# Kernel optimization log

Measured on AMD Instinct MI355X. Metric: run time of the kernel, lower is better.

Reference implementation:

```python
import jax, jax.numpy as jnp
import numpy as np

B, L, PATCH_IN, D, NPOS = 64, 1024, 768, 1152, 256


def setup_inputs() -> dict:
    key = jax.random.key(0)
    k1, k2, k3, k4 = jax.random.split(key, 4)
    pixel_values = jax.random.normal(k1, (B, L, PATCH_IN), dtype=jnp.float32)
    # per-sample (h, w) with h*w <= L and h, w >= 16 (pure upsampling of 16x16 grid)
    hs = np.array([16 + (i % 17) for i in range(B)], dtype=np.int64)
    ws = (L // hs).astype(np.int64)
    spatial_shapes = jnp.asarray(np.stack([hs, ws], axis=1))
    W = jax.random.normal(k2, (D, PATCH_IN), dtype=jnp.float32) * 0.02
    b = jax.random.normal(k3, (D,), dtype=jnp.float32) * 0.02
    pos_emb = jax.random.normal(k4, (NPOS, D), dtype=jnp.float32) * 0.02
    return {"pixel_values": pixel_values, "spatial_shapes": spatial_shapes,
            "W": W, "b": b, "pos_emb": pos_emb}


def _resized_pos_embeddings(pos_emb, spatial_shapes_np, max_length):
    # pos_emb: [num_patches, D] -> [G, G, D] grid
    g = int(np.sqrt(pos_emb.shape[0]))
    d = pos_emb.shape[1]
    grid = pos_emb.reshape(g, g, d)
    rows = []
    for i in range(spatial_shapes_np.shape[0]):
        h, w = int(spatial_shapes_np[i, 0]), int(spatial_shapes_np[i, 1])
        # half-pixel bilinear == torch F.interpolate(align_corners=False); antialias
        # is a no-op for upsampling (h, w >= g)
        r = jax.image.resize(grid, (h, w, d), method="bilinear").reshape(h * w, d)
        pad = jnp.broadcast_to(r[0], (max_length - h * w, d))  # replicate first patch
        rows.append(jnp.concatenate([r, pad], axis=0))
    return jnp.stack(rows)  # [B, max_length, D]


def reference(pixel_values, spatial_shapes, W, b, pos_emb):
    # patch linear embedding: [B, L, Cpp] x [D, Cpp] -> [B, L, D]
    patch_embeds = jnp.einsum("blk,dk->bld", pixel_values, W) + b
    ss = np.asarray(spatial_shapes)  # static per-sample shapes
    pos = _resized_pos_embeddings(pos_emb, ss, pixel_values.shape[1])
    return patch_embeds + pos
```

## Files before the change

### kernel.cpp

```cpp
#include <hip/hip_runtime.h>

typedef __bf16 bf16x8 __attribute__((ext_vector_type(8)));
typedef float  f32x4  __attribute__((ext_vector_type(4)));

constexpr int BM = 128, BN = 128, BK = 32;
constexpr int MDIM = 65536, NDIM = 1152, KDIM = 768;
constexpr int NBN = NDIM / BN;
constexpr int NKT = KDIM / BK;
constexpr int GRID = (MDIM / BM) * NBN;
constexpr int LDSROWB = BK * 2;

__device__ __forceinline__ void gload16(const void* g, void* l) {
  __builtin_amdgcn_global_load_lds(
      (const __attribute__((address_space(1))) void*)g,
      (__attribute__((address_space(3))) void*)l, 16, 0, 0);
}

__device__ __forceinline__ unsigned pk2(float x, float y) {
  __bf16 a = (__bf16)x, b = (__bf16)y;
  return (unsigned)__builtin_bit_cast(unsigned short, a) |
         ((unsigned)__builtin_bit_cast(unsigned short, b) << 16);
}

__device__ __forceinline__ void epilogue(const f32x4 acc[4][4], int bm, int bn,
                                         int wr, int wc, int lane,
                                         const int* __restrict__ ss,
                                         const float* __restrict__ bias,
                                         const float* __restrict__ pos,
                                         float* __restrict__ out) {
  const int fr = lane & 15;
  const int kg = lane >> 4;
  const int colbase = bn * BN + wc * 64 + fr;
  float bvals[4];
#pragma unroll
  for (int nf = 0; nf < 4; ++nf) bvals[nf] = bias[colbase + nf * 16];

  const int s  = bm >> 3;
  const int h  = ss[2 * s];
  const int w  = ss[2 * s + 1];
  const int hw = h * w;
  const float rh = 16.0f / (float)h;
  const float rw = 16.0f / (float)w;

  const int row0 = bm * BM + wr * 64 + kg * 4;

#pragma unroll
  for (int mf = 0; mf < 4; ++mf) {
#pragma unroll
    for (int rg = 0; rg < 4; ++rg) {
      const int row = row0 + mf * 16 + rg;
      int p = row & 1023;
      if (p >= hw) p = 0;
      const int y = p / w;
      const int x = p - y * w;
      const float fy = ((float)y + 0.5f) * rh - 0.5f;
      const float fx = ((float)x + 0.5f) * rw - 0.5f;
      const float yf = floorf(fy), xf = floorf(fx);
      const float ty = fy - yf,   tx = fx - xf;
      int iy0 = (int)yf, ix0 = (int)xf;
      int iy1 = iy0 + 1 > 15 ? 15 : iy0 + 1;
      int ix1 = ix0 + 1 > 15 ? 15 : ix0 + 1;
      iy0 = iy0 < 0 ? 0 : iy0;
      ix0 = ix0 < 0 ? 0 : ix0;
      const float* g00 = pos + (size_t)(iy0 * 16 + ix0) * NDIM;
      const float* g01 = pos + (size_t)(iy0 * 16 + ix1) * NDIM;
      const float* g10 = pos + (size_t)(iy1 * 16 + ix0) * NDIM;
      const float* g11 = pos + (size_t)(iy1 * 16 + ix1) * NDIM;
      float* orow = out + (size_t)row * NDIM;
#pragma unroll
      for (int nf = 0; nf < 4; ++nf) {
        const int col = colbase + nf * 16;
        const float p00 = g00[col], p01 = g01[col];
        const float p10 = g10[col], p11 = g11[col];
        const float top = p00 + tx * (p01 - p00);
        const float bot = p10 + tx * (p11 - p10);
        const float pv  = top + ty * (bot - top);
        orow[col] = acc[mf][nf][rg] + bvals[nf] + pv;
      }
    }
  }
}

__global__ __launch_bounds__(256)
void cvt_bf16_kernel(const float* __restrict__ in, __bf16* __restrict__ out, int n8) {
  int i = blockIdx.x * blockDim.x + threadIdx.x;
  const int stride = gridDim.x * blockDim.x;
  for (; i < n8; i += stride) {
    const float4 a = reinterpret_cast<const float4*>(in)[2 * i];
    const float4 b = reinterpret_cast<const float4*>(in)[2 * i + 1];
    bf16x8 r;
    r[0] = (__bf16)a.x; r[1] = (__bf16)a.y; r[2] = (__bf16)a.z; r[3] = (__bf16)a.w;
    r[4] = (__bf16)b.x; r[5] = (__bf16)b.y; r[6] = (__bf16)b.z; r[7] = (__bf16)b.w;
    reinterpret_cast<bf16x8*>(out)[i] = r;
  }
}

__global__ __launch_bounds__(256, 2)
void gemm_pre_kernel(const __bf16* __restrict__ Ab,
                     const __bf16* __restrict__ Bb,
                     const int*   __restrict__ ss,
                     const float* __restrict__ bias,
                     const float* __restrict__ pos,
                     float* __restrict__ out) {
  __shared__ __bf16 As[2][BM * BK];
  __shared__ __bf16 Bs[2][BM * BK];

  const int tid  = threadIdx.x;
  const int lane = tid & 63;
  const int wid  = tid >> 6;
  const int wr   = wid >> 1;
  const int wc   = wid & 1;

  const int bidh = blockIdx.x;
  const int bid  = (bidh & 7) * (GRID / 8) + (bidh >> 3);
  const int bm   = bid / NBN;
  const int bn   = bid % NBN;

  const __bf16* Abase = Ab + (size_t)bm * BM * KDIM;
  const __bf16* Bbase = Bb + (size_t)bn * BN * KDIM;

  auto stage = [&](int kt, int buf) {
    const int ko = kt * BK;
#pragma unroll
    for (int i = 0; i < 2; ++i) {
      const int c   = i * 256 + tid;
      const int row = c >> 2;
      const int prt = c & 3;
      gload16(Abase + (size_t)row * KDIM + ko + prt * 8,
              (char*)(&As[buf][0]) + c * 16);
      gload16(Bbase + (size_t)row * KDIM + ko + prt * 8,
              (char*)(&Bs[buf][0]) + c * 16);
    }
  };

  f32x4 acc[4][4];
#pragma unroll
  for (int i = 0; i < 4; ++i)
#pragma unroll
    for (int j = 0; j < 4; ++j) acc[i][j] = (f32x4)0.0f;

  const int fr = lane & 15;
  const int kg = lane >> 4;
  const int abase = (wr * 64 + fr) * LDSROWB + kg * 16;
  const int bbase = (wc * 64 + fr) * LDSROWB + kg * 16;

  auto compute = [&](int buf) {
    const char* pa = reinterpret_cast<const char*>(&As[buf][0]);
    const char* pb = reinterpret_cast<const char*>(&Bs[buf][0]);
    bf16x8 af[4], bfv[4];
#pragma unroll
    for (int mf = 0; mf < 4; ++mf)
      af[mf] = *reinterpret_cast<const bf16x8*>(pa + abase + mf * 16 * LDSROWB);
#pragma unroll
    for (int nf = 0; nf < 4; ++nf)
      bfv[nf] = *reinterpret_cast<const bf16x8*>(pb + bbase + nf * 16 * LDSROWB);
#pragma unroll
    for (int mf = 0; mf < 4; ++mf)
#pragma unroll
      for (int nf = 0; nf < 4; ++nf)
        acc[mf][nf] = __builtin_amdgcn_mfma_f32_16x16x32_bf16(af[mf], bfv[nf], acc[mf][nf], 0, 0, 0);
  };

  stage(0, 0);
  for (int kt = 0; kt < NKT; ++kt) {
    const int cur = kt & 1;
    __syncthreads();
    if (kt + 1 < NKT) stage(kt + 1, cur ^ 1);
    compute(cur);
  }

  epilogue(acc, bm, bn, wr, wc, lane, ss, bias, pos, out);
}

__global__ __launch_bounds__(256, 2)
void gemm_fb_kernel(const float* __restrict__ A,
                    const int*   __restrict__ ss,
                    const float* __restrict__ Wm,
                    const float* __restrict__ bias,
                    const float* __restrict__ pos,
                    float* __restrict__ out) {
  __shared__ unsigned short As[2][BM * BK];
  __shared__ unsigned short Bs[2][BM * BK];

  const int tid  = threadIdx.x;
  const int lane = tid & 63;
  const int wid  = tid >> 6;
  const int wr   = wid >> 1;
  const int wc   = wid & 1;

  const int bidh = blockIdx.x;
  const int bid  = (bidh & 7) * (GRID / 8) + (bidh >> 3);
  const int bm   = bid / NBN;
  const int bn   = bid % NBN;

  const int srow0 = tid >> 3;
  const int skc   = tid & 7;
  const float* Ag = A  + (size_t)(bm * BM + srow0) * KDIM + skc * 4;
  const float* Bg = Wm + (size_t)(bn * BN + srow0) * KDIM + skc * 4;

  float4 ra[4], rb[4];

  auto stage_load = [&](int kt) {
    const int ko = kt * BK;
#pragma unroll
    for (int r = 0; r < 4; ++r) {
      ra[r] = *reinterpret_cast<const float4*>(Ag + (size_t)(r * 32) * KDIM + ko);
      rb[r] = *reinterpret_cast<const float4*>(Bg + (size_t)(r * 32) * KDIM + ko);
    }
  };

  auto stage_write = [&](int buf) {
#pragma unroll
    for (int r = 0; r < 4; ++r) {
      const int arow = r * 32 + srow0;
      int off = arow * LDSROWB + skc * 8;
      off ^= (arow & 7) << 4;
      uint2 pa, pb;
      pa.x = pk2(ra[r].x, ra[r].y); pa.y = pk2(ra[r].z, ra[r].w);
      pb.x = pk2(rb[r].x, rb[r].y); pb.y = pk2(rb[r].z, rb[r].w);
      *reinterpret_cast<uint2*>(reinterpret_cast<char*>(&As[buf][0]) + off) = pa;
      *reinterpret_cast<uint2*>(reinterpret_cast<char*>(&Bs[buf][0]) + off) = pb;
    }
  };

  f32x4 acc[4][4];
#pragma unroll
  for (int i = 0; i < 4; ++i)
#pragma unroll
    for (int j = 0; j < 4; ++j) acc[i][j] = (f32x4)0.0f;

  const int fr = lane & 15;
  const int kg = lane >> 4;
  int abase = (wr * 64 + fr) * LDSROWB + kg * 16; abase ^= (fr & 7) << 4;
  int bbase = (wc * 64 + fr) * LDSROWB + kg * 16; bbase ^= (fr & 7) << 4;

  auto compute = [&](int buf) {
    const char* pa = reinterpret_cast<const char*>(&As[buf][0]);
    const char* pb = reinterpret_cast<const char*>(&Bs[buf][0]);
    bf16x8 af[4], bfv[4];
#pragma unroll
    for (int mf = 0; mf < 4; ++mf)
      af[mf] = *reinterpret_cast<const bf16x8*>(pa + abase + mf * 16 * LDSROWB);
#pragma unroll
    for (int nf = 0; nf < 4; ++nf)
      bfv[nf] = *reinterpret_cast<const bf16x8*>(pb + bbase + nf * 16 * LDSROWB);
#pragma unroll
    for (int mf = 0; mf < 4; ++mf)
#pragma unroll
      for (int nf = 0; nf < 4; ++nf)
        acc[mf][nf] = __builtin_amdgcn_mfma_f32_16x16x32_bf16(af[mf], bfv[nf], acc[mf][nf], 0, 0, 0);
  };

  stage_load(0);
  stage_write(0);
  for (int kt = 0; kt < NKT; ++kt) {
    const int cur = kt & 1;
    if (kt + 1 < NKT) stage_load(kt + 1);
    __syncthreads();
    compute(cur);
    if (kt + 1 < NKT) stage_write(cur ^ 1);
  }

  epilogue(acc, bm, bn, wr, wc, lane, ss, bias, pos, out);
}

extern "C" void kernel_launch(void* const* d_in, const int* in_sizes, int n_in,
                              void* d_out, int out_size, void* d_ws, size_t ws_size,
                              hipStream_t stream) {
  const float* A    = (const float*)d_in[0];
  const int*   ss   = (const int*)d_in[1];
  const float* Wm   = (const float*)d_in[2];
  const float* bias = (const float*)d_in[3];
  const float* pos  = (const float*)d_in[4];
  float* out = (float*)d_out;

  const size_t needA = (size_t)MDIM * KDIM * 2;
  const size_t needW = (size_t)NDIM * KDIM * 2;

  if (ws_size >= needA + needW) {
    __bf16* Ab = (__bf16*)d_ws;
    __bf16* Bb = (__bf16*)((char*)d_ws + needA);
    cvt_bf16_kernel<<<2048, 256, 0, stream>>>(A, Ab, MDIM * KDIM / 8);
    cvt_bf16_kernel<<<432, 256, 0, stream>>>(Wm, Bb, NDIM * KDIM / 8);
    gemm_pre_kernel<<<GRID, 256, 0, stream>>>(Ab, Bb, ss, bias, pos, out);
  } else {
    gemm_fb_kernel<<<GRID, 256, 0, stream>>>(A, ss, Wm, bias, pos, out);
  }
}
```

Before: 292.8 us.

## Pre-swizzle operands into MFMA fragment layout and load fragments directly from global

The bf16 conversion kernels now write A and W in a fragment-major layout that matches the 16x16x32 MFMA operand layout, so each lane reads its bf16x8 fragment with one contiguous 16-byte global load. The GEMM kernel drops LDS staging and __syncthreads entirely, using register double-buffering across k-tiles instead. This removes LDS traffic and barriers, but each wave now fetches its own operands from global or L2, with no sharing through LDS between the waves of a block. Performance then depends on cache hit rate and on how well load latency is hidden.

```diff
diff --git a/kernel.cpp b/kernel.cpp
--- a/kernel.cpp
+++ b/kernel.cpp
@@ -10,11 +10,7 @@
 constexpr int GRID = (MDIM / BM) * NBN;
 constexpr int LDSROWB = BK * 2;
 
-__device__ __forceinline__ void gload16(const void* g, void* l) {
-  __builtin_amdgcn_global_load_lds(
-      (const __attribute__((address_space(1))) void*)g,
-      (__attribute__((address_space(3))) void*)l, 16, 0, 0);
-}
+constexpr int RSTRIDE = NKT * 64 * 8;
 
 __device__ __forceinline__ unsigned pk2(float x, float y) {
   __bf16 a = (__bf16)x, b = (__bf16)y;
@@ -82,29 +78,29 @@
 }
 
 __global__ __launch_bounds__(256)
-void cvt_bf16_kernel(const float* __restrict__ in, __bf16* __restrict__ out, int n8) {
-  int i = blockIdx.x * blockDim.x + threadIdx.x;
-  const int stride = gridDim.x * blockDim.x;
-  for (; i < n8; i += stride) {
-    const float4 a = reinterpret_cast<const float4*>(in)[2 * i];
-    const float4 b = reinterpret_cast<const float4*>(in)[2 * i + 1];
-    bf16x8 r;
-    r[0] = (__bf16)a.x; r[1] = (__bf16)a.y; r[2] = (__bf16)a.z; r[3] = (__bf16)a.w;
-    r[4] = (__bf16)b.x; r[5] = (__bf16)b.y; r[6] = (__bf16)b.z; r[7] = (__bf16)b.w;
-    reinterpret_cast<bf16x8*>(out)[i] = r;
-  }
+void cvt_frag_kernel(const float* __restrict__ in, __bf16* __restrict__ out) {
+  const int c   = blockIdx.x * 256 + threadIdx.x;
+  const int fr  = c & 15;
+  const int kg  = (c >> 4) & 3;
+  const int ktR = c >> 6;
+  const int kt  = ktR % NKT;
+  const int R   = ktR / NKT;
+  const float* src = in + (size_t)(R * 16 + fr) * KDIM + kt * 32 + kg * 8;
+  const float4 a = *reinterpret_cast<const float4*>(src);
+  const float4 b = *reinterpret_cast<const float4*>(src + 4);
+  bf16x8 r;
+  r[0] = (__bf16)a.x; r[1] = (__bf16)a.y; r[2] = (__bf16)a.z; r[3] = (__bf16)a.w;
+  r[4] = (__bf16)b.x; r[5] = (__bf16)b.y; r[6] = (__bf16)b.z; r[7] = (__bf16)b.w;
+  *reinterpret_cast<bf16x8*>(out + (size_t)c * 8) = r;
 }
 
 __global__ __launch_bounds__(256, 2)
-void gemm_pre_kernel(const __bf16* __restrict__ Ab,
-                     const __bf16* __restrict__ Bb,
-                     const int*   __restrict__ ss,
-                     const float* __restrict__ bias,
-                     const float* __restrict__ pos,
-                     float* __restrict__ out) {
-  __shared__ __bf16 As[2][BM * BK];
-  __shared__ __bf16 Bs[2][BM * BK];
-
+void gemm_frag_kernel(const __bf16* __restrict__ Aw,
+                      const __bf16* __restrict__ Bw,
+                      const int*   __restrict__ ss,
+                      const float* __restrict__ bias,
+                      const float* __restrict__ pos,
+                      float* __restrict__ out) {
   const int tid  = threadIdx.x;
   const int lane = tid & 63;
   const int wid  = tid >> 6;
@@ -116,22 +112,8 @@
   const int bm   = bid / NBN;
   const int bn   = bid % NBN;
 
-  const __bf16* Abase = Ab + (size_t)bm * BM * KDIM;
-  const __bf16* Bbase = Bb + (size_t)bn * BN * KDIM;
-
-  auto stage = [&](int kt, int buf) {
-    const int ko = kt * BK;
-#pragma unroll
-    for (int i = 0; i < 2; ++i) {
-      const int c   = i * 256 + tid;
-      const int row = c >> 2;
-      const int prt = c & 3;
-      gload16(Abase + (size_t)row * KDIM + ko + prt * 8,
-              (char*)(&As[buf][0]) + c * 16);
-      gload16(Bbase + (size_t)row * KDIM + ko + prt * 8,
-              (char*)(&Bs[buf][0]) + c * 16);
-    }
-  };
+  const __bf16* pA = Aw + (size_t)(bm * 8 + wr * 4) * RSTRIDE + lane * 8;
+  const __bf16* pB = Bw + (size_t)(bn * 8 + wc * 4) * RSTRIDE + lane * 8;
 
   f32x4 acc[4][4];
 #pragma unroll
@@ -139,34 +121,33 @@
 #pragma unroll
     for (int j = 0; j < 4; ++j) acc[i][j] = (f32x4)0.0f;
 
-  const int fr = lane & 15;
-  const int kg = lane >> 4;
-  const int abase = (wr * 64 + fr) * LDSROWB + kg * 16;
-  const int bbase = (wc * 64 + fr) * LDSROWB + kg * 16;
-
-  auto compute = [&](int buf) {
-    const char* pa = reinterpret_cast<const char*>(&As[buf][0]);
-    const char* pb = reinterpret_cast<const char*>(&Bs[buf][0]);
-    bf16x8 af[4], bfv[4];
-#pragma unroll
-    for (int mf = 0; mf < 4; ++mf)
-      af[mf] = *reinterpret_cast<const bf16x8*>(pa + abase + mf * 16 * LDSROWB);
+  bf16x8 a0[4], b0[4], a1[4], b1[4];
+
+  auto lda = [&](bf16x8* d, int kt) {
+#pragma unroll
+    for (int mf = 0; mf < 4; ++mf)
+      d[mf] = *reinterpret_cast<const bf16x8*>(pA + mf * RSTRIDE + kt * 512);
+  };
+  auto ldb = [&](bf16x8* d, int kt) {
 #pragma unroll
     for (int nf = 0; nf < 4; ++nf)
-      bfv[nf] = *reinterpret_cast<const bf16x8*>(pb + bbase + nf * 16 * LDSROWB);
+      d[nf] = *reinterpret_cast<const bf16x8*>(pB + nf * RSTRIDE + kt * 512);
+  };
+  auto mm = [&](const bf16x8* a, const bf16x8* b) {
 #pragma unroll
     for (int mf = 0; mf < 4; ++mf)
 #pragma unroll
       for (int nf = 0; nf < 4; ++nf)
-        acc[mf][nf] = __builtin_amdgcn_mfma_f32_16x16x32_bf16(af[mf], bfv[nf], acc[mf][nf], 0, 0, 0);
-  };
-
-  stage(0, 0);
-  for (int kt = 0; kt < NKT; ++kt) {
-    const int cur = kt & 1;
-    __syncthreads();
-    if (kt + 1 < NKT) stage(kt + 1, cur ^ 1);
-    compute(cur);
+        acc[mf][nf] = __builtin_amdgcn_mfma_f32_16x16x32_bf16(a[mf], b[nf], acc[mf][nf], 0, 0, 0);
+  };
+
+  lda(a0, 0); ldb(b0, 0);
+#pragma unroll
+  for (int kt = 0; kt < NKT; kt += 2) {
+    lda(a1, kt + 1); ldb(b1, kt + 1);
+    mm(a0, b0);
+    if (kt + 2 < NKT) { lda(a0, kt + 2); ldb(b0, kt + 2); }
+    mm(a1, b1);
   }
 
   epilogue(acc, bm, bn, wr, wc, lane, ss, bias, pos, out);
@@ -280,9 +261,11 @@
   if (ws_size >= needA + needW) {
     __bf16* Ab = (__bf16*)d_ws;
     __bf16* Bb = (__bf16*)((char*)d_ws + needA);
-    cvt_bf16_kernel<<<2048, 256, 0, stream>>>(A, Ab, MDIM * KDIM / 8);
-    cvt_bf16_kernel<<<432, 256, 0, stream>>>(Wm, Bb, NDIM * KDIM / 8);
-    gemm_pre_kernel<<<GRID, 256, 0, stream>>>(Ab, Bb, ss, bias, pos, out);
+    const int chunksA = MDIM / 16 * NKT * 64;
+    const int chunksW = NDIM / 16 * NKT * 64;
+    cvt_frag_kernel<<<chunksA / 256, 256, 0, stream>>>(A, Ab);
+    cvt_frag_kernel<<<chunksW / 256, 256, 0, stream>>>(Wm, Bb);
+    gemm_frag_kernel<<<GRID, 256, 0, stream>>>(Ab, Bb, ss, bias, pos, out);
   } else {
     gemm_fb_kernel<<<GRID, 256, 0, stream>>>(A, ss, Wm, bias, pos, out);
   }
```

Result: slower. 365.1 us (+24.7%).

## Repack bf16 operands into pre-swizzled tile images for conflict-free LDS reads

Applied to the files above, without the earlier changes.

The fp32-to-bf16 conversion kernels now write A and W as contiguous 128x32 tile images with an XOR swizzle baked in. The GEMM can then stage each k-tile with fully contiguous 16-byte global-to-LDS loads, and its fragment reads use the matching XOR to avoid LDS bank conflicts. Launch bounds are raised to 3 blocks per SM to increase occupancy. The risks are register pressure at the higher occupancy and the repack kernel's strided, less coalesced reads of the fp32 input.

```diff
diff --git a/kernel.cpp b/kernel.cpp
--- a/kernel.cpp
+++ b/kernel.cpp
@@ -9,6 +9,7 @@
 constexpr int NKT = KDIM / BK;
 constexpr int GRID = (MDIM / BM) * NBN;
 constexpr int LDSROWB = BK * 2;
+
 
 __device__ __forceinline__ void gload16(const void* g, void* l) {
   __builtin_amdgcn_global_load_lds(
@@ -82,22 +83,30 @@
 }
 
 __global__ __launch_bounds__(256)
-void cvt_bf16_kernel(const float* __restrict__ in, __bf16* __restrict__ out, int n8) {
-  int i = blockIdx.x * blockDim.x + threadIdx.x;
-  const int stride = gridDim.x * blockDim.x;
-  for (; i < n8; i += stride) {
-    const float4 a = reinterpret_cast<const float4*>(in)[2 * i];
-    const float4 b = reinterpret_cast<const float4*>(in)[2 * i + 1];
-    bf16x8 r;
-    r[0] = (__bf16)a.x; r[1] = (__bf16)a.y; r[2] = (__bf16)a.z; r[3] = (__bf16)a.w;
-    r[4] = (__bf16)b.x; r[5] = (__bf16)b.y; r[6] = (__bf16)b.z; r[7] = (__bf16)b.w;
-    reinterpret_cast<bf16x8*>(out)[i] = r;
-  }
-}
-
-__global__ __launch_bounds__(256, 2)
-void gemm_pre_kernel(const __bf16* __restrict__ Ab,
-                     const __bf16* __restrict__ Bb,
+void repack_kernel(const float* __restrict__ in, __bf16* __restrict__ out) {
+  const int c    = blockIdx.x * 256 + threadIdx.x;
+  const int c_in = c & 511;
+  const int img  = c >> 9;
+  const int kt   = img % NKT;
+  const int pan  = img / NKT;
+  const int o = c_in * 16;
+  const int u = (o >> 6) & 7;
+  const int a = o ^ ((u ^ (u >> 2)) << 4);
+  const int r = a >> 6;
+  const int p = (a >> 4) & 3;
+  const float* src = in + (size_t)(pan * 128 + r) * KDIM + kt * 32 + p * 8;
+  const float4 x = *reinterpret_cast<const float4*>(src);
+  const float4 y = *reinterpret_cast<const float4*>(src + 4);
+  uint2 v0, v1;
+  v0.x = pk2(x.x, x.y); v0.y = pk2(x.z, x.w);
+  v1.x = pk2(y.x, y.y); v1.y = pk2(y.z, y.w);
+  uint4 r4; r4.x = v0.x; r4.y = v0.y; r4.z = v1.x; r4.w = v1.y;
+  *reinterpret_cast<uint4*>(out + (size_t)c * 8) = r4;
+}
+
+__global__ __launch_bounds__(256, 3)
+void gemm_swz_kernel(const __bf16* __restrict__ Aimg,
+                     const __bf16* __restrict__ Bimg,
                      const int*   __restrict__ ss,
                      const float* __restrict__ bias,
                      const float* __restrict__ pos,
@@ -116,21 +125,13 @@
   const int bm   = bid / NBN;
   const int bn   = bid % NBN;
 
-  const __bf16* Abase = Ab + (size_t)bm * BM * KDIM;
-  const __bf16* Bbase = Bb + (size_t)bn * BN * KDIM;
-
   auto stage = [&](int kt, int buf) {
-    const int ko = kt * BK;
-#pragma unroll
-    for (int i = 0; i < 2; ++i) {
-      const int c   = i * 256 + tid;
-      const int row = c >> 2;
-      const int prt = c & 3;
-      gload16(Abase + (size_t)row * KDIM + ko + prt * 8,
-              (char*)(&As[buf][0]) + c * 16);
-      gload16(Bbase + (size_t)row * KDIM + ko + prt * 8,
-              (char*)(&Bs[buf][0]) + c * 16);
-    }
+    const __bf16* wsA = Aimg + ((size_t)(bm * NKT + kt) << 12);
+    const __bf16* wsB = Bimg + ((size_t)(bn * NKT + kt) << 12);
+    gload16(wsA + tid * 8,         (char*)(&As[buf][0]) + tid * 16);
+    gload16(wsA + (256 + tid) * 8, (char*)(&As[buf][0]) + (256 + tid) * 16);
+    gload16(wsB + tid * 8,         (char*)(&Bs[buf][0]) + tid * 16);
+    gload16(wsB + (256 + tid) * 8, (char*)(&Bs[buf][0]) + (256 + tid) * 16);
   };
 
   f32x4 acc[4][4];
@@ -141,8 +142,8 @@
 
   const int fr = lane & 15;
   const int kg = lane >> 4;
-  const int abase = (wr * 64 + fr) * LDSROWB + kg * 16;
-  const int bbase = (wc * 64 + fr) * LDSROWB + kg * 16;
+  const int abase = (((wr * 64 + fr) * LDSROWB) + kg * 16) ^ ((fr & 7) << 4);
+  const int bbase = (((wc * 64 + fr) * LDSROWB) + kg * 16) ^ ((fr & 7) << 4);
 
   auto compute = [&](int buf) {
     const char* pa = reinterpret_cast<const char*>(&As[buf][0]);
@@ -280,9 +281,11 @@
   if (ws_size >= needA + needW) {
     __bf16* Ab = (__bf16*)d_ws;
     __bf16* Bb = (__bf16*)((char*)d_ws + needA);
-    cvt_bf16_kernel<<<2048, 256, 0, stream>>>(A, Ab, MDIM * KDIM / 8);
-    cvt_bf16_kernel<<<432, 256, 0, stream>>>(Wm, Bb, NDIM * KDIM / 8);
-    gemm_pre_kernel<<<GRID, 256, 0, stream>>>(Ab, Bb, ss, bias, pos, out);
+    const int chunksA = (MDIM / 16) * NKT * 64;
+    const int chunksW = (NDIM / 16) * NKT * 64;
+    repack_kernel<<<chunksA / 256, 256, 0, stream>>>(A, Ab);
+    repack_kernel<<<chunksW / 256, 256, 0, stream>>>(Wm, Bb);
+    gemm_swz_kernel<<<GRID, 256, 0, stream>>>(Ab, Bb, ss, bias, pos, out);
   } else {
     gemm_fb_kernel<<<GRID, 256, 0, stream>>>(A, ss, Wm, bias, pos, out);
   }
```

New measurement: 283.8 us. 3.1% less time.
